# Kernel optimization log

Measured on AMD Instinct MI355X. Metric: run time of the kernel, lower is better.

The kernel has to match this reference:

```python
import jax, jax.numpy as jnp
import numpy as np

N_NODES = 10000
N_EDGES = 160000
IN_FEATS = 512
HEADS = 8
OUT_FEATS = 64
NEG_SLOPE = 0.2


def setup_inputs() -> dict:
    key = jax.random.key(0)
    k_feat, k_w, k_al, k_ar, k_src, k_dst = jax.random.split(key, 6)
    feat = jax.random.normal(k_feat, (N_NODES, IN_FEATS), dtype=jnp.float32)
    # fc weight stored as [in_feats, heads*out_feats] (x @ W == Linear without bias)
    W = jax.random.normal(k_w, (IN_FEATS, HEADS * OUT_FEATS), dtype=jnp.float32) * 0.05
    attn_l = jax.random.normal(k_al, (HEADS, OUT_FEATS), dtype=jnp.float32) * 0.1
    attn_r = jax.random.normal(k_ar, (HEADS, OUT_FEATS), dtype=jnp.float32) * 0.1
    bias = jnp.zeros((HEADS * OUT_FEATS,), dtype=jnp.float32)
    src = jax.random.randint(k_src, (N_EDGES,), 0, N_NODES, dtype=jnp.int32)
    dst = jax.random.randint(k_dst, (N_EDGES,), 0, N_NODES, dtype=jnp.int32)
    return {"feat": feat, "W": W, "attn_l": attn_l, "attn_r": attn_r,
            "bias": bias, "src": src, "dst": dst}


def reference(feat, W, attn_l, attn_r, bias, src, dst):
    # 1) project features: [N, H, F]
    h = (feat @ W).reshape(N_NODES, HEADS, OUT_FEATS)
    # 2) per-node attention logits: el_i = a_l . h_i, er_j = a_r . h_j  -> [N, H]
    el = jnp.einsum('nhf,hf->nh', h, attn_l)
    er = jnp.einsum('nhf,hf->nh', h, attn_r)
    # 3) edge scores: u_add_v + LeakyReLU  -> [E, H]
    e = el[src] + er[dst]
    e = jnp.where(e > 0, e, NEG_SLOPE * e)
    # 4) edge softmax over incoming edges of each destination node
    m = jax.ops.segment_max(e, dst, num_segments=N_NODES)  # [N, H]
    a = jnp.exp(e - m[dst])
    s = jax.ops.segment_sum(a, dst, num_segments=N_NODES)  # [N, H]
    a = a / s[dst]
    # 5) weighted scatter-sum aggregation: sum_j a_ij * h_j  -> [N, H, F]
    msg = h[src] * a[:, :, None]                           # [E, H, F]
    rst = jax.ops.segment_sum(msg, dst, num_segments=N_NODES)
    # 6) bias
    rst = rst + bias.reshape(1, HEADS, OUT_FEATS)
    return rst
```

## Files before the change

### kernel.cpp

```cpp
#include <hip/hip_runtime.h>
#include <math.h>

#define N_NODES 10000
#define N_EDGES 160000
#define IN_FEATS 512
#define HEADS 8
#define OUT_FEATS 64
#define HF 512
#define NEG_SLOPE 0.2f
#define M_PAD 10048
#define MAXDEG 64

typedef float  f32x4  __attribute__((ext_vector_type(4)));
typedef __bf16 bf16x8 __attribute__((ext_vector_type(8)));
typedef short  s16x8  __attribute__((ext_vector_type(8)));

__device__ __forceinline__ unsigned short f2bf_rn(float x) {
    unsigned u = __float_as_uint(x);
    unsigned r = u + 0x7FFFu + ((u >> 16) & 1u);
    return (unsigned short)(r >> 16);
}

__device__ __forceinline__ void gl_lds16(const void* g, void* l) {
    __builtin_amdgcn_global_load_lds((const __attribute__((address_space(1))) void*)g,
                                     (__attribute__((address_space(3))) void*)l, 16, 0, 0);
}

#define SF_BLOCKS 5024
#define PW_BLOCKS 64
#define Z_BLOCKS  10
__global__ __launch_bounds__(256) void prep2_kernel(const float* __restrict__ feat,
                                                    const float* __restrict__ W,
                                                    unsigned short* __restrict__ Abf,
                                                    unsigned short* __restrict__ Bt,
                                                    int* __restrict__ counts) {
    __shared__ float tile[64][65];
    const int bid = blockIdx.x;
    const int tid = threadIdx.x;

    if (bid < SF_BLOCKS) {
        const int idx = bid * 256 + tid;
        const int row = idx >> 7;
        const int c4  = idx & 127;
        float4 v = make_float4(0.f, 0.f, 0.f, 0.f);
        if (row < N_NODES)
            v = *reinterpret_cast<const float4*>(feat + (size_t)row * IN_FEATS + c4 * 4);
        ushort4 o;
        o.x = f2bf_rn(v.x);
        o.y = f2bf_rn(v.y);
        o.z = f2bf_rn(v.z);
        o.w = f2bf_rn(v.w);
        *reinterpret_cast<ushort4*>(Abf + (size_t)row * IN_FEATS + c4 * 4) = o;
    } else if (bid < SF_BLOCKS + PW_BLOCKS) {
        const int b2 = bid - SF_BLOCKS;
        const int k0 = (b2 & 7) * 64;
        const int n0 = (b2 >> 3) * 64;
        #pragma unroll
        for (int i = 0; i < 4; ++i) {
            int f = tid + 256 * i;
            int r = f >> 4, c4 = f & 15;
            float4 v = *reinterpret_cast<const float4*>(W + (size_t)(k0 + r) * HF + n0 + c4 * 4);
            tile[r][c4 * 4 + 0] = v.x;
            tile[r][c4 * 4 + 1] = v.y;
            tile[r][c4 * 4 + 2] = v.z;
            tile[r][c4 * 4 + 3] = v.w;
        }
        __syncthreads();
        #pragma unroll
        for (int i = 0; i < 4; ++i) {
            int f = tid + 256 * i;
            int rn = f >> 4, c4 = f & 15;
            ushort4 o;
            o.x = f2bf_rn(tile[c4 * 4 + 0][rn]);
            o.y = f2bf_rn(tile[c4 * 4 + 1][rn]);
            o.z = f2bf_rn(tile[c4 * 4 + 2][rn]);
            o.w = f2bf_rn(tile[c4 * 4 + 3][rn]);
            *reinterpret_cast<ushort4*>(Bt + (size_t)(n0 + rn) * IN_FEATS + k0 + c4 * 4) = o;
        }
    } else {
        const int idx = (bid - SF_BLOCKS - PW_BLOCKS) * 256 + tid;
        if (idx < N_NODES / 4)
            reinterpret_cast<int4*>(counts)[idx] = make_int4(0, 0, 0, 0);
    }
}

#define GTM 64
#define GTN 128
#define GBK 32
#define GY   (M_PAD / GTM)
#define HIST_Y 157
__global__ __launch_bounds__(256) void gemm_mfma(const unsigned short* __restrict__ Abf,
                                                 const unsigned short* __restrict__ Bt,
                                                 const float* __restrict__ attn_l,
                                                 const float* __restrict__ attn_r,
                                                 const int* __restrict__ src,
                                                 const int* __restrict__ dst,
                                                 int* __restrict__ counts,
                                                 int* __restrict__ ssrc2,
                                                 unsigned short* __restrict__ hbf,
                                                 float* __restrict__ el,
                                                 float* __restrict__ er) {
    __shared__ unsigned short sA[2][GTM * GBK];
    __shared__ unsigned short sB[2][GTN * GBK];

    if (blockIdx.y >= GY) {
        const int he = (blockIdx.y - GY) * (HF / GTN) + blockIdx.x;
        const int e  = he * 256 + threadIdx.x;
        if (e < N_EDGES) {
            const int d = dst[e];
            const int o = atomicAdd(&counts[d], 1);
            if (o < MAXDEG) ssrc2[(d << 6) + o] = src[e];
        }
        return;
    }

    const int tid  = threadIdx.x;
    const int lane = tid & 63;
    const int w    = tid >> 6;
    const int wm   = w >> 1, wn = w & 1;
    const int m16  = lane & 15, quad = lane >> 4;
    const int row0 = blockIdx.y * GTM;
    const int col0 = blockIdx.x * GTN;
    const int hh   = blockIdx.x * 2 + wn;

    const int srow  = lane >> 2;
    const int kperm = ((lane & 3) ^ ((lane >> 4) & 3)) * 8;

    f32x4 acc[2][4] = {};

    auto stage = [&](int nb, int k0) {
        #pragma unroll
        for (int jj = 0; jj < 3; ++jj) {
            const int j = w * 3 + jj;
            if (j < 4) {
                const unsigned short* g = Abf
                    + (size_t)(row0 + j * 16 + srow) * IN_FEATS + k0 + kperm;
                gl_lds16(g, &sA[nb][j * 512]);
            } else {
                const int ch = j - 4;
                const unsigned short* g = Bt
                    + (size_t)(col0 + ch * 16 + srow) * IN_FEATS + k0 + kperm;
                gl_lds16(g, &sB[nb][ch * 512]);
            }
        }
    };

    stage(0, 0);
    int nb = 0;
    const int asw = (quad ^ ((m16 >> 2) & 3)) * 8;

    for (int kt = 0; kt < 16; ++kt) {
        __syncthreads();
        if (kt < 15) stage(nb ^ 1, (kt + 1) * GBK);

        s16x8 fa[2], fb[4];
        #pragma unroll
        for (int mi = 0; mi < 2; ++mi)
            fa[mi] = *reinterpret_cast<const s16x8*>(&sA[nb][(wm * 2 + mi) * 512 + m16 * 32 + asw]);
        #pragma unroll
        for (int ni = 0; ni < 4; ++ni)
            fb[ni] = *reinterpret_cast<const s16x8*>(&sB[nb][(wn * 4 + ni) * 512 + m16 * 32 + asw]);
        #pragma unroll
        for (int mi = 0; mi < 2; ++mi)
            #pragma unroll
            for (int ni = 0; ni < 4; ++ni)
                acc[mi][ni] = __builtin_amdgcn_mfma_f32_16x16x32_bf16(
                    __builtin_bit_cast(bf16x8, fa[mi]), __builtin_bit_cast(bf16x8, fb[ni]),
                    acc[mi][ni], 0, 0, 0);
        nb ^= 1;
    }

    float alw[4], arw[4];
    #pragma unroll
    for (int ni = 0; ni < 4; ++ni) {
        alw[ni] = attn_l[hh * OUT_FEATS + ni * 16 + m16];
        arw[ni] = attn_r[hh * OUT_FEATS + ni * 16 + m16];
    }
    #pragma unroll
    for (int mi = 0; mi < 2; ++mi) {
        #pragma unroll
        for (int r = 0; r < 4; ++r) {
            const int row = row0 + wm * 32 + mi * 16 + quad * 4 + r;
            if (row < N_NODES) {
                float pl = 0.f, pr = 0.f;
                #pragma unroll
                for (int ni = 0; ni < 4; ++ni) {
                    const float v = acc[mi][ni][r];
                    hbf[(size_t)row * HF + hh * OUT_FEATS + ni * 16 + m16] = f2bf_rn(v);
                    pl = fmaf(v, alw[ni], pl);
                    pr = fmaf(v, arw[ni], pr);
                }
                #pragma unroll
                for (int off = 1; off < 16; off <<= 1) {
                    pl += __shfl_xor(pl, off);
                    pr += __shfl_xor(pr, off);
                }
                if (m16 == 0) {
                    el[row * HEADS + hh] = pl;
                    er[row * HEADS + hh] = pr;
                }
            }
        }
    }
}

__global__ __launch_bounds__(256) void aggregate_kernel(const unsigned short* __restrict__ hbf,
                                                        const float* __restrict__ el,
                                                        const float* __restrict__ er,
                                                        const float* __restrict__ bias,
                                                        const int* __restrict__ counts,
                                                        const int* __restrict__ ssrc2,
                                                        float* __restrict__ out) {
    const int n    = (blockIdx.x * 256 + threadIdx.x) >> 6;
    const int lane = threadIdx.x & 63;
    if (n >= N_NODES) return;
    const int head = lane >> 3;
    const int deg  = counts[n];

    float4 b0 = *reinterpret_cast<const float4*>(bias + lane * 8);
    float4 b1 = *reinterpret_cast<const float4*>(bias + lane * 8 + 4);
    float* op = out + (size_t)n * HF + lane * 8;
    if (deg == 0) {
        *reinterpret_cast<float4*>(op)     = b0;
        *reinterpret_cast<float4*>(op + 4) = b1;
        return;
    }

    const int* __restrict__ sp = ssrc2 + (n << 6);
    const unsigned short* __restrict__ hb = hbf + lane * 8;
    const float erv = er[n * 8 + head];

    float acc[8] = {};
    float s = 0.f;

    for (int k = 0; k < deg; k += 8) {
        const int nb = (deg - k < 8) ? (deg - k) : 8;
        int sx[8]; float elv[8]; uint4 u[8];
        #pragma unroll
        for (int j = 0; j < 8; ++j) {
            const int kk = k + j;
            sx[j] = sp[(kk < deg) ? kk : 0];
        }
        #pragma unroll
        for (int j = 0; j < 8; ++j)
            elv[j] = el[sx[j] * 8 + head];
        #pragma unroll
        for (int j = 0; j < 8; ++j)
            u[j] = *reinterpret_cast<const uint4*>(hb + (size_t)sx[j] * HF);
        #pragma unroll
        for (int j = 0; j < 8; ++j) {
            const unsigned* wp = (const unsigned*)&u[j];
            float x = elv[j] + erv;
            float v = x > 0.f ? x : NEG_SLOPE * x;
            float p = __expf(v);
            if (j >= nb) p = 0.f;
            s += p;
            #pragma unroll
            for (int q = 0; q < 4; ++q) {
                acc[2 * q]     = fmaf(p, __uint_as_float(wp[q] << 16),         acc[2 * q]);
                acc[2 * q + 1] = fmaf(p, __uint_as_float(wp[q] & 0xFFFF0000u), acc[2 * q + 1]);
            }
        }
    }

    const float inv = 1.0f / s;
    float4 o0 = make_float4(acc[0] * inv + b0.x, acc[1] * inv + b0.y,
                            acc[2] * inv + b0.z, acc[3] * inv + b0.w);
    float4 o1 = make_float4(acc[4] * inv + b1.x, acc[5] * inv + b1.y,
                            acc[6] * inv + b1.z, acc[7] * inv + b1.w);
    *reinterpret_cast<float4*>(op)     = o0;
    *reinterpret_cast<float4*>(op + 4) = o1;
}

extern "C" void kernel_launch(void* const* d_in, const int* in_sizes, int n_in,
                              void* d_out, int out_size, void* d_ws, size_t ws_size,
                              hipStream_t stream) {
    const float* feat   = (const float*)d_in[0];
    const float* W      = (const float*)d_in[1];
    const float* attn_l = (const float*)d_in[2];
    const float* attn_r = (const float*)d_in[3];
    const float* bias   = (const float*)d_in[4];
    const int*   src    = (const int*)d_in[5];
    const int*   dst    = (const int*)d_in[6];
    float* out = (float*)d_out;

    char* ws = (char*)d_ws;
    unsigned short* Abf    = (unsigned short*)ws; ws += (size_t)M_PAD * IN_FEATS * 2;
    unsigned short* Bt     = (unsigned short*)ws; ws += (size_t)IN_FEATS * HF * 2;
    unsigned short* hbf    = (unsigned short*)ws; ws += (size_t)N_NODES * HF * 2;
    float*          el_buf = (float*)ws;          ws += (size_t)N_NODES * HEADS * 4;
    float*          er_buf = (float*)ws;          ws += (size_t)N_NODES * HEADS * 4;
    int*            ssrc2  = (int*)ws;            ws += (size_t)(N_NODES + 1) * MAXDEG * 4;
    int*            counts = (int*)ws;            ws += (size_t)N_NODES * 4;

    prep2_kernel<<<SF_BLOCKS + PW_BLOCKS + Z_BLOCKS, 256, 0, stream>>>(
        feat, W, Abf, Bt, counts);

    dim3 ggrid(HF / GTN, GY + HIST_Y);
    gemm_mfma<<<ggrid, 256, 0, stream>>>(Abf, Bt, attn_l, attn_r,
                                         src, dst, counts, ssrc2,
                                         hbf, el_buf, er_buf);

    aggregate_kernel<<<(N_NODES * 64 + 255) / 256, 256, 0, stream>>>(
        hbf, el_buf, er_buf, bias, counts, ssrc2, out);
}
```

Baseline: 132.9 us.

## Store projected features head-major and aggregate per head with edge-parallel lanes

The GEMM epilogue now writes the bf16 projected features in a [head][node][feat] layout, so each head's features form a compact 10000x64 slab. The aggregation kernel is split so that each block handles one head for four destination nodes. Within a wave, 8 lane groups each process different incoming edges in parallel, and partial sums are combined with cross-lane shuffles. This is meant to improve cache locality of gathers within a head and to expose more parallelism per node. The cost is a shuffle reduction, repeated reads of the index list and logits per head, and more blocks.

```diff
diff --git a/kernel.cpp b/kernel.cpp
--- a/kernel.cpp
+++ b/kernel.cpp
@@ -186,7 +186,7 @@
                 #pragma unroll
                 for (int ni = 0; ni < 4; ++ni) {
                     const float v = acc[mi][ni][r];
-                    hbf[(size_t)row * HF + hh * OUT_FEATS + ni * 16 + m16] = f2bf_rn(v);
+                    hbf[((size_t)hh * N_NODES + row) * OUT_FEATS + ni * 16 + m16] = f2bf_rn(v);
                     pl = fmaf(v, alw[ni], pl);
                     pr = fmaf(v, arw[ni], pr);
                 }
@@ -204,72 +204,87 @@
     }
 }
 
-__global__ __launch_bounds__(256) void aggregate_kernel(const unsigned short* __restrict__ hbf,
-                                                        const float* __restrict__ el,
-                                                        const float* __restrict__ er,
-                                                        const float* __restrict__ bias,
-                                                        const int* __restrict__ counts,
-                                                        const int* __restrict__ ssrc2,
-                                                        float* __restrict__ out) {
-    const int n    = (blockIdx.x * 256 + threadIdx.x) >> 6;
+__global__ __launch_bounds__(256) void aggregate2_kernel(const unsigned short* __restrict__ hbf,
+                                                         const float* __restrict__ el,
+                                                         const float* __restrict__ er,
+                                                         const float* __restrict__ bias,
+                                                         const int* __restrict__ counts,
+                                                         const int* __restrict__ ssrc2,
+                                                         float* __restrict__ out) {
+    const int bid  = blockIdx.x;
+    const int head = bid & 7;
+    const int nb4  = bid >> 3;
+    const int wv   = threadIdx.x >> 6;
     const int lane = threadIdx.x & 63;
+    const int n    = nb4 * 4 + wv;
     if (n >= N_NODES) return;
-    const int head = lane >> 3;
-    const int deg  = counts[n];
-
-    float4 b0 = *reinterpret_cast<const float4*>(bias + lane * 8);
-    float4 b1 = *reinterpret_cast<const float4*>(bias + lane * 8 + 4);
-    float* op = out + (size_t)n * HF + lane * 8;
+    const int g  = lane >> 3;
+    const int lf = lane & 7;
+
+    float* op = out + (size_t)n * HF + head * OUT_FEATS + lf * 8;
+    const float4 bb0 = *reinterpret_cast<const float4*>(bias + head * OUT_FEATS + lf * 8);
+    const float4 bb1 = *reinterpret_cast<const float4*>(bias + head * OUT_FEATS + lf * 8 + 4);
+
+    const int deg = counts[n];
     if (deg == 0) {
-        *reinterpret_cast<float4*>(op)     = b0;
-        *reinterpret_cast<float4*>(op + 4) = b1;
+        if (g == 0) {
+            *reinterpret_cast<float4*>(op)     = bb0;
+            *reinterpret_cast<float4*>(op + 4) = bb1;
+        }
         return;
     }
 
     const int* __restrict__ sp = ssrc2 + (n << 6);
-    const unsigned short* __restrict__ hb = hbf + lane * 8;
+    const unsigned short* __restrict__ hb = hbf + ((size_t)head * N_NODES << 6) + lf * 8;
     const float erv = er[n * 8 + head];
 
     float acc[8] = {};
     float s = 0.f;
 
-    for (int k = 0; k < deg; k += 8) {
-        const int nb = (deg - k < 8) ? (deg - k) : 8;
-        int sx[8]; float elv[8]; uint4 u[8];
-        #pragma unroll
-        for (int j = 0; j < 8; ++j) {
-            const int kk = k + j;
-            sx[j] = sp[(kk < deg) ? kk : 0];
-        }
-        #pragma unroll
-        for (int j = 0; j < 8; ++j)
-            elv[j] = el[sx[j] * 8 + head];
-        #pragma unroll
-        for (int j = 0; j < 8; ++j)
-            u[j] = *reinterpret_cast<const uint4*>(hb + (size_t)sx[j] * HF);
-        #pragma unroll
-        for (int j = 0; j < 8; ++j) {
-            const unsigned* wp = (const unsigned*)&u[j];
-            float x = elv[j] + erv;
-            float v = x > 0.f ? x : NEG_SLOPE * x;
-            float p = __expf(v);
-            if (j >= nb) p = 0.f;
-            s += p;
-            #pragma unroll
-            for (int q = 0; q < 4; ++q) {
-                acc[2 * q]     = fmaf(p, __uint_as_float(wp[q] << 16),         acc[2 * q]);
-                acc[2 * q + 1] = fmaf(p, __uint_as_float(wp[q] & 0xFFFF0000u), acc[2 * q + 1]);
-            }
-        }
-    }
-
-    const float inv = 1.0f / s;
-    float4 o0 = make_float4(acc[0] * inv + b0.x, acc[1] * inv + b0.y,
-                            acc[2] * inv + b0.z, acc[3] * inv + b0.w);
-    float4 o1 = make_float4(acc[4] * inv + b1.x, acc[5] * inv + b1.y,
-                            acc[6] * inv + b1.z, acc[7] * inv + b1.w);
-    *reinterpret_cast<float4*>(op)     = o0;
-    *reinterpret_cast<float4*>(op + 4) = o1;
+    for (int k = 0; k < deg; k += 16) {
+        const int e0 = k + g, e1 = k + 8 + g;
+        float p0 = 0.f, p1 = 0.f;
+        uint4 u0 = make_uint4(0u, 0u, 0u, 0u), u1 = make_uint4(0u, 0u, 0u, 0u);
+        if (e0 < deg) {
+            const int sx = sp[e0];
+            u0 = *reinterpret_cast<const uint4*>(hb + ((size_t)sx << 6));
+            const float x = el[sx * 8 + head] + erv;
+            p0 = __expf(x > 0.f ? x : NEG_SLOPE * x);
+        }
+        if (e1 < deg) {
+            const int sx = sp[e1];
+            u1 = *reinterpret_cast<const uint4*>(hb + ((size_t)sx << 6));
+            const float x = el[sx * 8 + head] + erv;
+            p1 = __expf(x > 0.f ? x : NEG_SLOPE * x);
+        }
+        s += p0 + p1;
+        const unsigned* w0 = (const unsigned*)&u0;
+        const unsigned* w1 = (const unsigned*)&u1;
+        #pragma unroll
+        for (int q = 0; q < 4; ++q) {
+            acc[2 * q]     = fmaf(p0, __uint_as_float(w0[q] << 16),         acc[2 * q]);
+            acc[2 * q + 1] = fmaf(p0, __uint_as_float(w0[q] & 0xFFFF0000u), acc[2 * q + 1]);
+            acc[2 * q]     = fmaf(p1, __uint_as_float(w1[q] << 16),         acc[2 * q]);
+            acc[2 * q + 1] = fmaf(p1, __uint_as_float(w1[q] & 0xFFFF0000u), acc[2 * q + 1]);
+        }
+    }
+
+    #pragma unroll
+    for (int off = 8; off < 64; off <<= 1) {
+        s += __shfl_xor(s, off);
+        #pragma unroll
+        for (int j = 0; j < 8; ++j) acc[j] += __shfl_xor(acc[j], off);
+    }
+
+    if (g == 0) {
+        const float inv = 1.0f / s;
+        float4 o0 = make_float4(acc[0] * inv + bb0.x, acc[1] * inv + bb0.y,
+                                acc[2] * inv + bb0.z, acc[3] * inv + bb0.w);
+        float4 o1 = make_float4(acc[4] * inv + bb1.x, acc[5] * inv + bb1.y,
+                                acc[6] * inv + bb1.z, acc[7] * inv + bb1.w);
+        *reinterpret_cast<float4*>(op)     = o0;
+        *reinterpret_cast<float4*>(op + 4) = o1;
+    }
 }
 
 extern "C" void kernel_launch(void* const* d_in, const int* in_sizes, int n_in,
@@ -287,7 +302,7 @@
     char* ws = (char*)d_ws;
     unsigned short* Abf    = (unsigned short*)ws; ws += (size_t)M_PAD * IN_FEATS * 2;
     unsigned short* Bt     = (unsigned short*)ws; ws += (size_t)IN_FEATS * HF * 2;
-    unsigned short* hbf    = (unsigned short*)ws; ws += (size_t)N_NODES * HF * 2;
+    unsigned short* hbf    = (unsigned short*)ws; ws += (size_t)HEADS * N_NODES * OUT_FEATS * 2;
     float*          el_buf = (float*)ws;          ws += (size_t)N_NODES * HEADS * 4;
     float*          er_buf = (float*)ws;          ws += (size_t)N_NODES * HEADS * 4;
     int*            ssrc2  = (int*)ws;            ws += (size_t)(N_NODES + 1) * MAXDEG * 4;
@@ -301,6 +316,6 @@
                                          src, dst, counts, ssrc2,
                                          hbf, el_buf, er_buf);
 
-    aggregate_kernel<<<(N_NODES * 64 + 255) / 256, 256, 0, stream>>>(
+    aggregate2_kernel<<<((N_NODES + 3) / 4) * HEADS, 256, 0, stream>>>(
         hbf, el_buf, er_buf, bias, counts, ssrc2, out);
 }
```

New measurement: 143.3 us. 1.08x slower.
